# Optimization experiments

Hardware: AMD Instinct MI355X
Metric: run time of the kernel (lower is better)

Reference implementation:

```python
import jax, jax.numpy as jnp
import numpy as np

N_USERS = 200_000
N_ITEMS = 100_000
EMB = 64
N_EDGES = 5_000_000
N_LAYERS = 3


def setup_inputs() -> dict:
    key = jax.random.key(0)
    k1, k2, k3, k4, k5 = jax.random.split(key, 5)
    emb_user = jax.random.normal(k1, (N_USERS, EMB), dtype=jnp.float32) * 0.1
    emb_item = jax.random.normal(k2, (N_ITEMS, EMB), dtype=jnp.float32) * 0.1
    n_nodes = N_USERS + N_ITEMS
    edge_row = jax.random.randint(k3, (N_EDGES,), 0, n_nodes, dtype=jnp.int32)
    edge_col = jax.random.randint(k4, (N_EDGES,), 0, n_nodes, dtype=jnp.int32)
    # normalized adjacency values (positive, < 1), stand-in for D^-1/2 A D^-1/2
    edge_val = jax.random.uniform(k5, (N_EDGES,), dtype=jnp.float32)
    return {"emb_user": emb_user, "emb_item": emb_item,
            "edge_val": edge_val, "edge_row": edge_row, "edge_col": edge_col}


def reference(emb_user, emb_item, edge_val, edge_row, edge_col):
    n_users = emb_user.shape[0]
    n_nodes = n_users + emb_item.shape[0]
    # 0th-layer embedding matrix: cat(user, item)  [N, D]
    x = jnp.concatenate([emb_user, emb_item], axis=0)
    layers = [x]
    for _ in range(N_LAYERS):
        # SpMM: out[r] += val * x[c] for each edge (r, c)
        x = jax.ops.segment_sum(edge_val[:, None] * x[edge_col], edge_row,
                                num_segments=n_nodes)
        layers.append(x)
    # layer combination: mean over all layers
    agg = jnp.mean(jnp.stack(layers, axis=0), axis=0)
    return agg[:n_users], agg[n_users:]
```

## Files before the change

### kernel.cpp

```cpp
#include <hip/hip_runtime.h>

#define N_USERS 200000
#define N_ITEMS 100000
#define N_NODES 300000
#define EMB     64
#define N_EDGES 5000000

typedef float f32x4 __attribute__((ext_vector_type(4)));
typedef _Float16 f16;
typedef f16 f16x4 __attribute__((ext_vector_type(4)));

struct alignas(8) SRec { unsigned int rc; float val; };

#define BSHIFT 10
#define BROWS  (1 << BSHIFT)
#define NBUCK  ((N_NODES + BROWS - 1) >> BSHIFT)
#define CAP    20000
#define BIN_CHUNK 16384
#define BIN_THREADS 1024
#define COLMASK 0x7FFFFu
#define INIT_BLOCKS 512

__global__ __launch_bounds__(1024) void fused_init_bin_kernel(
    const float* __restrict__ user, const float* __restrict__ item,
    f16* __restrict__ x0,
    const int4* __restrict__ row4, const int4* __restrict__ col4,
    const float4* __restrict__ val4,
    int* __restrict__ bcursor, SRec* __restrict__ stage, int bin_blocks)
{
    int t = threadIdx.x;
    if ((int)blockIdx.x < bin_blocks) {
        __shared__ int hist[NBUCK];
        __shared__ int base_[NBUCK];
        const int Q = N_EDGES / 4;
        long q0 = (long)blockIdx.x * (BIN_CHUNK / 4);

        for (int k = t; k < NBUCK; k += BIN_THREADS) hist[k] = 0;
        __syncthreads();

        int4 ra[4];
        const bool full = (q0 + (BIN_CHUNK / 4) <= Q);
        if (full) {
            #pragma unroll
            for (int k = 0; k < 4; ++k)
                ra[k] = row4[q0 + k * BIN_THREADS + t];
            #pragma unroll
            for (int k = 0; k < 4; ++k) {
                atomicAdd(&hist[ra[k].x >> BSHIFT], 1);
                atomicAdd(&hist[ra[k].y >> BSHIFT], 1);
                atomicAdd(&hist[ra[k].z >> BSHIFT], 1);
                atomicAdd(&hist[ra[k].w >> BSHIFT], 1);
            }
        } else {
            #pragma unroll
            for (int k = 0; k < 4; ++k) {
                long q = q0 + k * BIN_THREADS + t;
                if (q < Q) {
                    ra[k] = row4[q];
                    atomicAdd(&hist[ra[k].x >> BSHIFT], 1);
                    atomicAdd(&hist[ra[k].y >> BSHIFT], 1);
                    atomicAdd(&hist[ra[k].z >> BSHIFT], 1);
                    atomicAdd(&hist[ra[k].w >> BSHIFT], 1);
                }
            }
        }
        __syncthreads();
        for (int k = t; k < NBUCK; k += BIN_THREADS) {
            int h = hist[k];
            base_[k] = h ? atomicAdd(&bcursor[k], h) : 0;
            hist[k] = 0;
        }
        __syncthreads();
        int4 c4[4]; float4 v4[4];
        if (full) {
            #pragma unroll
            for (int k = 0; k < 4; ++k) {
                c4[k] = col4[q0 + k * BIN_THREADS + t];
                v4[k] = val4[q0 + k * BIN_THREADS + t];
            }
        } else {
            #pragma unroll
            for (int k = 0; k < 4; ++k) {
                long q = q0 + k * BIN_THREADS + t;
                if (q < Q) { c4[k] = col4[q]; v4[k] = val4[q]; }
            }
        }
        #pragma unroll
        for (int k = 0; k < 4; ++k) {
            long q = q0 + k * BIN_THREADS + t;
            if (full || q < Q) {
                int   rr[4] = {ra[k].x, ra[k].y, ra[k].z, ra[k].w};
                int   cc[4] = {c4[k].x, c4[k].y, c4[k].z, c4[k].w};
                float vv[4] = {v4[k].x, v4[k].y, v4[k].z, v4[k].w};
                #pragma unroll
                for (int m = 0; m < 4; ++m) {
                    int b   = rr[m] >> BSHIFT;
                    int pos = base_[b] + atomicAdd(&hist[b], 1);
                    SRec s;
                    s.rc  = ((unsigned)(rr[m] & (BROWS - 1)) << 19)
                          | (unsigned)cc[m];
                    s.val = vv[m];
                    stage[(size_t)b * CAP + pos] = s;
                }
            }
        }
    } else {
        const int nu4 = N_USERS * EMB / 4;
        const int nt4 = N_NODES * EMB / 4;
        int i0 = ((int)blockIdx.x - bin_blocks) * BIN_THREADS + t;
        const int stride = INIT_BLOCKS * BIN_THREADS;
        for (int i = i0; i < nt4; i += stride) {
            float4 vv = (i < nu4) ? reinterpret_cast<const float4*>(user)[i]
                                  : reinterpret_cast<const float4*>(item)[i - nu4];
            f16x4 hx = {(f16)vv.x, (f16)vv.y, (f16)vv.z, (f16)vv.w};
            reinterpret_cast<f16x4*>(x0)[i] = hx;
        }
    }
}

__global__ __launch_bounds__(1024) void bucket_scan_scatter_kernel(
    const SRec* __restrict__ stage, const int* __restrict__ bsize,
    int* __restrict__ start, unsigned short* __restrict__ cnt16,
    int* __restrict__ pcol, f16* __restrict__ pval)
{
    __shared__ int cur[BROWS];
    __shared__ int sc[1024];
    __shared__ int lcol[CAP];
    __shared__ f16 lval[CAP];

    int b    = blockIdx.x;
    int t    = threadIdx.x;
    int row0 = b << BSHIFT;
    int rows = N_NODES - row0; if (rows > BROWS) rows = BROWS;

    const int  size = bsize[b];
    const int  base = b * CAP;
    const SRec* seg = stage + (size_t)b * CAP;

    cur[t] = 0;
    __syncthreads();

    for (int e = t; e < size; e += 1024)
        atomicAdd(&cur[seg[e].rc >> 19], 1);
    __syncthreads();

    int a = cur[t];
    sc[t] = a;
    __syncthreads();
    for (int ofs = 1; ofs < 1024; ofs <<= 1) {
        int v = (t >= ofs) ? sc[t - ofs] : 0;
        __syncthreads();
        sc[t] += v;
        __syncthreads();
    }
    int excl = sc[t] - a;
    cur[t] = excl;
    if (t < rows) {
        start[row0 + t] = base + excl;
        cnt16[row0 + t] = (unsigned short)a;
    }
    __syncthreads();

    for (int e = t; e < size; e += 1024) {
        SRec srec = seg[e];
        int idx = atomicAdd(&cur[srec.rc >> 19], 1);
        lcol[idx] = (int)(srec.rc & COLMASK);
        lval[idx] = (f16)srec.val;
    }
    __syncthreads();

    for (int i = t; i < size; i += 1024) pcol[base + i] = lcol[i];
    for (int i = t; i < size; i += 1024) pval[base + i] = lval[i];
}

__global__ __launch_bounds__(256, 4) void spmm_csr_kernel(
    const f16* __restrict__ x, const int* __restrict__ pcol,
    const f16* __restrict__ pval, const int* __restrict__ start,
    const unsigned short* __restrict__ cnt16,
    f16* __restrict__ y,
    const f16* __restrict__ xa, const f16* __restrict__ xb,
    float* __restrict__ out, int mode)
{
    int g = blockIdx.x * (256 / 16) + (threadIdx.x >> 4);
    if (g >= N_NODES) return;
    const int lane16 = threadIdx.x & 15;
    const int d      = lane16 * 4;
    const int gbase  = threadIdx.x & 48;

    int beg = start[g];
    int end = beg + cnt16[g];
    float4 acc = {0.f, 0.f, 0.f, 0.f};

    for (int jb = beg; jb < end; jb += 16) {
        int   mycol = 0; float myval = 0.f;
        if (jb + lane16 < end) {
            mycol = pcol[jb + lane16];
            myval = (float)pval[jb + lane16];
        }

        int   cols[16];
        float vals[16];
        #pragma unroll
        for (int k = 0; k < 16; ++k) {
            cols[k] = __shfl(mycol, gbase + k, 64);
            vals[k] = __shfl(myval, gbase + k, 64);
        }

        f16x4 xv[16];
        #pragma unroll
        for (int k = 0; k < 16; ++k) {
            xv[k] = *reinterpret_cast<const f16x4*>(
                x + (size_t)cols[k] * EMB + d);
        }

        #pragma unroll
        for (int k = 0; k < 16; ++k) {
            acc.x += vals[k] * (float)xv[k].x;
            acc.y += vals[k] * (float)xv[k].y;
            acc.z += vals[k] * (float)xv[k].z;
            acc.w += vals[k] * (float)xv[k].w;
        }
    }

    const size_t rofs = (size_t)g * EMB + d;
    if (mode == 0) {
        f16x4 hy = {(f16)acc.x, (f16)acc.y, (f16)acc.z, (f16)acc.w};
        *reinterpret_cast<f16x4*>(y + rofs) = hy;
    } else {
        f16x4 v0 = *reinterpret_cast<const f16x4*>(xa + rofs);
        f16x4 v1 = *reinterpret_cast<const f16x4*>(xb + rofs);
        f16x4 v2 = *reinterpret_cast<const f16x4*>(x  + rofs);
        f32x4 o;
        o.x = 0.25f * ((float)v0.x + (float)v1.x + (float)v2.x + acc.x);
        o.y = 0.25f * ((float)v0.y + (float)v1.y + (float)v2.y + acc.y);
        o.z = 0.25f * ((float)v0.z + (float)v1.z + (float)v2.z + acc.z);
        o.w = 0.25f * ((float)v0.w + (float)v1.w + (float)v2.w + acc.w);
        __builtin_nontemporal_store(o, reinterpret_cast<f32x4*>(out + rofs));
    }
}

__global__ __launch_bounds__(256) void init_kernel(
    const float* __restrict__ user, const float* __restrict__ item,
    float* __restrict__ x, float* __restrict__ out)
{
    const int nu4 = N_USERS * EMB / 4;
    const int nt4 = N_NODES * EMB / 4;
    int i = blockIdx.x * blockDim.x + threadIdx.x;
    if (i >= nt4) return;
    float4 v = (i < nu4) ? reinterpret_cast<const float4*>(user)[i]
                         : reinterpret_cast<const float4*>(item)[i - nu4];
    reinterpret_cast<float4*>(x)[i]   = v;
    reinterpret_cast<float4*>(out)[i] = v;
}

__global__ __launch_bounds__(256) void spmm_atomic_kernel(
    const float* __restrict__ x, const float* __restrict__ val,
    const int* __restrict__ row, const int* __restrict__ col,
    float* __restrict__ y)
{
    int t = blockIdx.x * blockDim.x + threadIdx.x;
    int e = t >> 4;
    if (e >= N_EDGES) return;
    int d = (t & 15) * 4;
    int   r = row[e];
    int   c = col[e];
    float v = val[e];
    float4 xv = *reinterpret_cast<const float4*>(x + c * EMB + d);
    float* yp = y + r * EMB + d;
    unsafeAtomicAdd(yp + 0, v * xv.x);
    unsafeAtomicAdd(yp + 1, v * xv.y);
    unsafeAtomicAdd(yp + 2, v * xv.z);
    unsafeAtomicAdd(yp + 3, v * xv.w);
}

__global__ __launch_bounds__(256) void addscale_kernel(
    const float* __restrict__ xl, float* __restrict__ out, float scale)
{
    const int nt4 = N_NODES * EMB / 4;
    int i = blockIdx.x * blockDim.x + threadIdx.x;
    if (i >= nt4) return;
    float4 a = reinterpret_cast<float4*>(out)[i];
    float4 b = reinterpret_cast<const float4*>(xl)[i];
    a.x = (a.x + b.x) * scale;
    a.y = (a.y + b.y) * scale;
    a.z = (a.z + b.z) * scale;
    a.w = (a.w + b.w) * scale;
    reinterpret_cast<float4*>(out)[i] = a;
}

extern "C" void kernel_launch(void* const* d_in, const int* in_sizes, int n_in,
                              void* d_out, int out_size, void* d_ws, size_t ws_size,
                              hipStream_t stream) {
    const float* emb_user = (const float*)d_in[0];
    const float* emb_item = (const float*)d_in[1];
    const float* edge_val = (const float*)d_in[2];
    const int*   edge_row = (const int*)d_in[3];
    const int*   edge_col = (const int*)d_in[4];
    float* out = (float*)d_out;

    const size_t node_elems = (size_t)N_NODES * EMB;
    char* ws = (char*)d_ws;

    const size_t off_bufA    = 0;
    const size_t off_bufB    = off_bufA + node_elems * sizeof(float);
    const size_t off_pcol    = off_bufB + node_elems * sizeof(float);
    const size_t off_pval    = off_pcol + (size_t)NBUCK * CAP * sizeof(int);
    const size_t off_start   = off_pval + (size_t)NBUCK * CAP * sizeof(f16);
    const size_t off_cnt16   = off_start + (N_NODES + 4) * sizeof(int);
    const size_t off_bcursor = off_cnt16 + (N_NODES + 4) * sizeof(unsigned short);
    const size_t needed      = off_bcursor + (NBUCK + 4) * sizeof(int);

    const int nt4       = N_NODES * EMB / 4;
    const int el_blocks = (nt4 + 255) / 256;
    const int e_blocks  = (N_EDGES + 255) / 256;

    static_assert((size_t)NBUCK * CAP * sizeof(SRec) <= (size_t)N_NODES * EMB * sizeof(float),
                  "stage must fit in bufB region");

    if (ws_size >= needed) {
        f16*  x0buf   = (f16*) (ws + off_bufA);
        f16*  x2buf   = (f16*) (ws + off_bufA) + node_elems;
        f16*  x1buf   = (f16*) (ws + off_bufB);
        int*  pcol    = (int*) (ws + off_pcol);
        f16*  pval    = (f16*) (ws + off_pval);
        int*  start   = (int*) (ws + off_start);
        unsigned short* cnt16 = (unsigned short*)(ws + off_cnt16);
        int*  bcursor = (int*) (ws + off_bcursor);
        SRec* stage   = (SRec*)(ws + off_bufB);

        hipMemsetAsync(bcursor, 0, (NBUCK + 4) * sizeof(int), stream);

        const int bin_blocks = (N_EDGES + BIN_CHUNK - 1) / BIN_CHUNK;
        fused_init_bin_kernel<<<bin_blocks + INIT_BLOCKS, BIN_THREADS, 0, stream>>>(
            emb_user, emb_item, x0buf,
            (const int4*)edge_row, (const int4*)edge_col, (const float4*)edge_val,
            bcursor, stage, bin_blocks);

        bucket_scan_scatter_kernel<<<NBUCK, 1024, 0, stream>>>(
            stage, bcursor, start, cnt16, pcol, pval);

        const int row_blocks = (N_NODES + 15) / 16;
        spmm_csr_kernel<<<row_blocks, 256, 0, stream>>>(
            x0buf, pcol, pval, start, cnt16, x1buf, nullptr, nullptr, nullptr, 0);
        spmm_csr_kernel<<<row_blocks, 256, 0, stream>>>(
            x1buf, pcol, pval, start, cnt16, x2buf, nullptr, nullptr, nullptr, 0);
        spmm_csr_kernel<<<row_blocks, 256, 0, stream>>>(
            x2buf, pcol, pval, start, cnt16, nullptr, x0buf, x1buf, out, 1);
    } else {
        float* fbufA = (float*)(ws + off_bufA);
        float* fbufB = (float*)(ws + off_bufB);
        init_kernel<<<el_blocks, 256, 0, stream>>>(emb_user, emb_item, fbufA, out);
        const int ew_blocks = (N_EDGES * 16 + 255) / 256;
        float* cur = fbufA;
        float* nxt = fbufB;
        for (int layer = 0; layer < 3; ++layer) {
            hipMemsetAsync(nxt, 0, node_elems * sizeof(float), stream);
            spmm_atomic_kernel<<<ew_blocks, 256, 0, stream>>>(
                cur, edge_val, edge_row, edge_col, nxt);
            addscale_kernel<<<el_blocks, 256, 0, stream>>>(
                nxt, out, (layer == 2) ? 0.25f : 1.0f);
            float* tmp = cur; cur = nxt; nxt = tmp;
        }
    }
}
```

Baseline: 549.6 us.

## Stage binned edges in shared memory for coalesced bucket writes

Measured after the change: 530.9 us. 3.4% less time.

```diff
diff --git a/kernel.cpp b/kernel.cpp
--- a/kernel.cpp
+++ b/kernel.cpp
@@ -30,10 +30,16 @@
 {
     int t = threadIdx.x;
     if ((int)blockIdx.x < bin_blocks) {
-        __shared__ int hist[NBUCK];
-        __shared__ int base_[NBUCK];
+        __shared__ int  hist[NBUCK];
+        __shared__ int  lstart[NBUCK + 1];
+        __shared__ int  gbase[NBUCK];
+        __shared__ int  sc[512];
+        __shared__ SRec sbuf[BIN_CHUNK];
+
         const int Q = N_EDGES / 4;
         long q0 = (long)blockIdx.x * (BIN_CHUNK / 4);
+        int  csize = N_EDGES - (int)(q0 * 4);
+        if (csize > BIN_CHUNK) csize = BIN_CHUNK;
 
         for (int k = t; k < NBUCK; k += BIN_THREADS) hist[k] = 0;
         __syncthreads();
@@ -65,12 +71,26 @@
             }
         }
         __syncthreads();
-        for (int k = t; k < NBUCK; k += BIN_THREADS) {
-            int h = hist[k];
-            base_[k] = h ? atomicAdd(&bcursor[k], h) : 0;
-            hist[k] = 0;
-        }
-        __syncthreads();
+
+        int v = (t < NBUCK) ? hist[t] : 0;
+        if (t < 512) sc[t] = v;
+        __syncthreads();
+        for (int ofs = 1; ofs < 512; ofs <<= 1) {
+            int u = 0;
+            if (t < 512 && t >= ofs) u = sc[t - ofs];
+            __syncthreads();
+            if (t < 512) sc[t] += u;
+            __syncthreads();
+        }
+        if (t < NBUCK) lstart[t] = sc[t] - v;
+        if (t == NBUCK - 1) lstart[NBUCK] = sc[t];
+        __syncthreads();
+        if (t < NBUCK) {
+            gbase[t] = v ? atomicAdd(&bcursor[t], v) : 0;
+            hist[t]  = lstart[t];
+        }
+        __syncthreads();
+
         int4 c4[4]; float4 v4[4];
         if (full) {
             #pragma unroll
@@ -95,14 +115,24 @@
                 #pragma unroll
                 for (int m = 0; m < 4; ++m) {
                     int b   = rr[m] >> BSHIFT;
-                    int pos = base_[b] + atomicAdd(&hist[b], 1);
+                    int idx = atomicAdd(&hist[b], 1);
                     SRec s;
                     s.rc  = ((unsigned)(rr[m] & (BROWS - 1)) << 19)
                           | (unsigned)cc[m];
                     s.val = vv[m];
-                    stage[(size_t)b * CAP + pos] = s;
+                    sbuf[idx] = s;
                 }
             }
+        }
+        __syncthreads();
+
+        for (int i = t; i < csize; i += BIN_THREADS) {
+            int lo = 0, hi = NBUCK - 1;
+            while (lo < hi) {
+                int mid = (lo + hi + 1) >> 1;
+                if (lstart[mid] <= i) lo = mid; else hi = mid - 1;
+            }
+            stage[(size_t)lo * CAP + gbase[lo] + (i - lstart[lo])] = sbuf[i];
         }
     } else {
         const int nu4 = N_USERS * EMB / 4;
```

## Locally sort edges in shared memory before coalesced bucket staging writes

Applied to the files above, without the earlier changes.

Measured after the change: 524.9 us. -4.5%, faster.

```diff
diff --git a/kernel.cpp b/kernel.cpp
--- a/kernel.cpp
+++ b/kernel.cpp
@@ -10,142 +10,152 @@
 typedef _Float16 f16;
 typedef f16 f16x4 __attribute__((ext_vector_type(4)));
 
-struct alignas(8) SRec { unsigned int rc; float val; };
-
-#define BSHIFT 10
-#define BROWS  (1 << BSHIFT)
-#define NBUCK  ((N_NODES + BROWS - 1) >> BSHIFT)
-#define CAP    20000
-#define BIN_CHUNK 16384
-#define BIN_THREADS 1024
+#define NBUCK  256
+#define BROWS  1172
+#define CAP    20800
 #define COLMASK 0x7FFFFu
-#define INIT_BLOCKS 512
+
+#define BIN_CHUNK 19532
+#define BIN_Q     (BIN_CHUNK / 4)
 
 __global__ __launch_bounds__(1024) void fused_init_bin_kernel(
     const float* __restrict__ user, const float* __restrict__ item,
     f16* __restrict__ x0,
     const int4* __restrict__ row4, const int4* __restrict__ col4,
     const float4* __restrict__ val4,
-    int* __restrict__ bcursor, SRec* __restrict__ stage, int bin_blocks)
-{
-    int t = threadIdx.x;
-    if ((int)blockIdx.x < bin_blocks) {
-        __shared__ int hist[NBUCK];
-        __shared__ int base_[NBUCK];
-        const int Q = N_EDGES / 4;
-        long q0 = (long)blockIdx.x * (BIN_CHUNK / 4);
-
-        for (int k = t; k < NBUCK; k += BIN_THREADS) hist[k] = 0;
+    int* __restrict__ bcursor,
+    unsigned int* __restrict__ stage_rc, f16* __restrict__ stage_val)
+{
+    __shared__ unsigned int lrc[BIN_CHUNK];
+    __shared__ f16          lv[BIN_CHUNK];
+    __shared__ int hist[NBUCK];
+    __shared__ int lstart[NBUCK + 1];
+    __shared__ int gbase[NBUCK];
+    __shared__ int sc[NBUCK];
+
+    const int t = threadIdx.x;
+    const int b = blockIdx.x;
+    const int Q    = N_EDGES / 4;
+    const int q0   = b * BIN_Q;
+    int qend = q0 + BIN_Q; if (qend > Q) qend = Q;
+    const int csize = (qend - q0) * 4;
+
+    for (int k = t; k < NBUCK; k += 1024) hist[k] = 0;
+    __syncthreads();
+
+    int4 ra[5]; bool ok[5];
+    #pragma unroll
+    for (int k = 0; k < 5; ++k) {
+        int q = q0 + k * 1024 + t;
+        ok[k] = (q < qend);
+        if (ok[k]) ra[k] = row4[q];
+    }
+    #pragma unroll
+    for (int k = 0; k < 5; ++k) {
+        if (ok[k]) {
+            atomicAdd(&hist[ra[k].x / BROWS], 1);
+            atomicAdd(&hist[ra[k].y / BROWS], 1);
+            atomicAdd(&hist[ra[k].z / BROWS], 1);
+            atomicAdd(&hist[ra[k].w / BROWS], 1);
+        }
+    }
+    __syncthreads();
+
+    if (t < NBUCK) sc[t] = hist[t];
+    __syncthreads();
+    for (int ofs = 1; ofs < NBUCK; ofs <<= 1) {
+        int u = 0;
+        if (t < NBUCK && t >= ofs) u = sc[t - ofs];
         __syncthreads();
-
-        int4 ra[4];
-        const bool full = (q0 + (BIN_CHUNK / 4) <= Q);
-        if (full) {
+        if (t < NBUCK) sc[t] += u;
+        __syncthreads();
+    }
+    if (t < NBUCK) {
+        int v  = hist[t];
+        int ex = sc[t] - v;
+        lstart[t] = ex;
+        gbase[t]  = v ? atomicAdd(&bcursor[t], v) : 0;
+        hist[t]   = ex;
+    }
+    if (t == 0) lstart[NBUCK] = csize;
+    __syncthreads();
+
+    int4 c4[5]; float4 v4[5];
+    #pragma unroll
+    for (int k = 0; k < 5; ++k) {
+        int q = q0 + k * 1024 + t;
+        if (ok[k]) { c4[k] = col4[q]; v4[k] = val4[q]; }
+    }
+    #pragma unroll
+    for (int k = 0; k < 5; ++k) {
+        if (ok[k]) {
+            int   rr[4] = {ra[k].x, ra[k].y, ra[k].z, ra[k].w};
+            int   cc[4] = {c4[k].x, c4[k].y, c4[k].z, c4[k].w};
+            float vv[4] = {v4[k].x, v4[k].y, v4[k].z, v4[k].w};
             #pragma unroll
-            for (int k = 0; k < 4; ++k)
-                ra[k] = row4[q0 + k * BIN_THREADS + t];
-            #pragma unroll
-            for (int k = 0; k < 4; ++k) {
-                atomicAdd(&hist[ra[k].x >> BSHIFT], 1);
-                atomicAdd(&hist[ra[k].y >> BSHIFT], 1);
-                atomicAdd(&hist[ra[k].z >> BSHIFT], 1);
-                atomicAdd(&hist[ra[k].w >> BSHIFT], 1);
+            for (int m = 0; m < 4; ++m) {
+                int bb    = rr[m] / BROWS;
+                int local = rr[m] - bb * BROWS;
+                int idx   = atomicAdd(&hist[bb], 1);
+                lrc[idx]  = ((unsigned)local << 19) | (unsigned)cc[m];
+                lv[idx]   = (f16)vv[m];
             }
-        } else {
-            #pragma unroll
-            for (int k = 0; k < 4; ++k) {
-                long q = q0 + k * BIN_THREADS + t;
-                if (q < Q) {
-                    ra[k] = row4[q];
-                    atomicAdd(&hist[ra[k].x >> BSHIFT], 1);
-                    atomicAdd(&hist[ra[k].y >> BSHIFT], 1);
-                    atomicAdd(&hist[ra[k].z >> BSHIFT], 1);
-                    atomicAdd(&hist[ra[k].w >> BSHIFT], 1);
-                }
-            }
-        }
-        __syncthreads();
-        for (int k = t; k < NBUCK; k += BIN_THREADS) {
-            int h = hist[k];
-            base_[k] = h ? atomicAdd(&bcursor[k], h) : 0;
-            hist[k] = 0;
-        }
-        __syncthreads();
-        int4 c4[4]; float4 v4[4];
-        if (full) {
-            #pragma unroll
-            for (int k = 0; k < 4; ++k) {
-                c4[k] = col4[q0 + k * BIN_THREADS + t];
-                v4[k] = val4[q0 + k * BIN_THREADS + t];
-            }
-        } else {
-            #pragma unroll
-            for (int k = 0; k < 4; ++k) {
-                long q = q0 + k * BIN_THREADS + t;
-                if (q < Q) { c4[k] = col4[q]; v4[k] = val4[q]; }
-            }
-        }
-        #pragma unroll
-        for (int k = 0; k < 4; ++k) {
-            long q = q0 + k * BIN_THREADS + t;
-            if (full || q < Q) {
-                int   rr[4] = {ra[k].x, ra[k].y, ra[k].z, ra[k].w};
-                int   cc[4] = {c4[k].x, c4[k].y, c4[k].z, c4[k].w};
-                float vv[4] = {v4[k].x, v4[k].y, v4[k].z, v4[k].w};
-                #pragma unroll
-                for (int m = 0; m < 4; ++m) {
-                    int b   = rr[m] >> BSHIFT;
-                    int pos = base_[b] + atomicAdd(&hist[b], 1);
-                    SRec s;
-                    s.rc  = ((unsigned)(rr[m] & (BROWS - 1)) << 19)
-                          | (unsigned)cc[m];
-                    s.val = vv[m];
-                    stage[(size_t)b * CAP + pos] = s;
-                }
-            }
-        }
-    } else {
-        const int nu4 = N_USERS * EMB / 4;
-        const int nt4 = N_NODES * EMB / 4;
-        int i0 = ((int)blockIdx.x - bin_blocks) * BIN_THREADS + t;
-        const int stride = INIT_BLOCKS * BIN_THREADS;
-        for (int i = i0; i < nt4; i += stride) {
-            float4 vv = (i < nu4) ? reinterpret_cast<const float4*>(user)[i]
-                                  : reinterpret_cast<const float4*>(item)[i - nu4];
-            f16x4 hx = {(f16)vv.x, (f16)vv.y, (f16)vv.z, (f16)vv.w};
-            reinterpret_cast<f16x4*>(x0)[i] = hx;
-        }
+        }
+    }
+    __syncthreads();
+
+    for (int i = t; i < csize; i += 1024) {
+        int lo = 0, hi = NBUCK - 1;
+        while (lo < hi) {
+            int mid = (lo + hi + 1) >> 1;
+            if (lstart[mid] <= i) lo = mid; else hi = mid - 1;
+        }
+        size_t gp = (size_t)lo * CAP + gbase[lo] + (i - lstart[lo]);
+        stage_rc[gp]  = lrc[i];
+        stage_val[gp] = lv[i];
+    }
+
+    const int nu4 = N_USERS * EMB / 4;
+    const int nt4 = N_NODES * EMB / 4;
+    for (int i = b * 1024 + t; i < nt4; i += NBUCK * 1024) {
+        float4 vv = (i < nu4) ? reinterpret_cast<const float4*>(user)[i]
+                              : reinterpret_cast<const float4*>(item)[i - nu4];
+        f16x4 hx = {(f16)vv.x, (f16)vv.y, (f16)vv.z, (f16)vv.w};
+        reinterpret_cast<f16x4*>(x0)[i] = hx;
     }
 }
 
 __global__ __launch_bounds__(1024) void bucket_scan_scatter_kernel(
-    const SRec* __restrict__ stage, const int* __restrict__ bsize,
+    const unsigned int* __restrict__ stage_rc, const f16* __restrict__ stage_val,
+    const int* __restrict__ bsize,
     int* __restrict__ start, unsigned short* __restrict__ cnt16,
     int* __restrict__ pcol, f16* __restrict__ pval)
 {
-    __shared__ int cur[BROWS];
+    __shared__ int cur[BROWS + 2];
     __shared__ int sc[1024];
     __shared__ int lcol[CAP];
     __shared__ f16 lval[CAP];
 
     int b    = blockIdx.x;
     int t    = threadIdx.x;
-    int row0 = b << BSHIFT;
+    int row0 = b * BROWS;
     int rows = N_NODES - row0; if (rows > BROWS) rows = BROWS;
 
-    const int  size = bsize[b];
-    const int  base = b * CAP;
-    const SRec* seg = stage + (size_t)b * CAP;
-
-    cur[t] = 0;
+    const int size = bsize[b];
+    const int base = b * CAP;
+    const unsigned int* seg_rc = stage_rc  + (size_t)b * CAP;
+    const f16*          seg_v  = stage_val + (size_t)b * CAP;
+
+    for (int i = t; i < BROWS; i += 1024) cur[i] = 0;
     __syncthreads();
 
     for (int e = t; e < size; e += 1024)
-        atomicAdd(&cur[seg[e].rc >> 19], 1);
-    __syncthreads();
-
-    int a = cur[t];
-    sc[t] = a;
+        atomicAdd(&cur[seg_rc[e] >> 19], 1);
+    __syncthreads();
+
+    int a0 = 0, a1 = 0, s01 = 0;
+    if (t < 586) { a0 = cur[2 * t]; a1 = cur[2 * t + 1]; s01 = a0 + a1; }
+    sc[t] = s01;
     __syncthreads();
     for (int ofs = 1; ofs < 1024; ofs <<= 1) {
         int v = (t >= ofs) ? sc[t - ofs] : 0;
@@ -153,19 +163,21 @@
         sc[t] += v;
         __syncthreads();
     }
-    int excl = sc[t] - a;
-    cur[t] = excl;
-    if (t < rows) {
-        start[row0 + t] = base + excl;
-        cnt16[row0 + t] = (unsigned short)a;
+    if (t < 586) {
+        int ex = sc[t] - s01;
+        cur[2 * t]     = ex;
+        cur[2 * t + 1] = ex + a0;
+        int r0 = 2 * t, r1 = 2 * t + 1;
+        if (r0 < rows) { start[row0 + r0] = base + ex;      cnt16[row0 + r0] = (unsigned short)a0; }
+        if (r1 < rows) { start[row0 + r1] = base + ex + a0; cnt16[row0 + r1] = (unsigned short)a1; }
     }
     __syncthreads();
 
     for (int e = t; e < size; e += 1024) {
-        SRec srec = seg[e];
-        int idx = atomicAdd(&cur[srec.rc >> 19], 1);
-        lcol[idx] = (int)(srec.rc & COLMASK);
-        lval[idx] = (f16)srec.val;
+        unsigned int rc = seg_rc[e];
+        int idx = atomicAdd(&cur[rc >> 19], 1);
+        lcol[idx] = (int)(rc & COLMASK);
+        lval[idx] = seg_v[e];
     }
     __syncthreads();
 
@@ -299,45 +311,46 @@
     float* out = (float*)d_out;
 
     const size_t node_elems = (size_t)N_NODES * EMB;
+    const size_t SEG        = (size_t)NBUCK * CAP;
     char* ws = (char*)d_ws;
 
     const size_t off_bufA    = 0;
     const size_t off_bufB    = off_bufA + node_elems * sizeof(float);
     const size_t off_pcol    = off_bufB + node_elems * sizeof(float);
-    const size_t off_pval    = off_pcol + (size_t)NBUCK * CAP * sizeof(int);
-    const size_t off_start   = off_pval + (size_t)NBUCK * CAP * sizeof(f16);
+    const size_t off_pval    = off_pcol + SEG * sizeof(int);
+    const size_t off_start   = off_pval + SEG * sizeof(f16);
     const size_t off_cnt16   = off_start + (N_NODES + 4) * sizeof(int);
     const size_t off_bcursor = off_cnt16 + (N_NODES + 4) * sizeof(unsigned short);
     const size_t needed      = off_bcursor + (NBUCK + 4) * sizeof(int);
 
     const int nt4       = N_NODES * EMB / 4;
     const int el_blocks = (nt4 + 255) / 256;
-    const int e_blocks  = (N_EDGES + 255) / 256;
-
-    static_assert((size_t)NBUCK * CAP * sizeof(SRec) <= (size_t)N_NODES * EMB * sizeof(float),
+
+    static_assert(SEG * 6 <= (size_t)N_NODES * EMB * sizeof(float),
                   "stage must fit in bufB region");
+    static_assert((size_t)NBUCK * BROWS >= N_NODES, "buckets must cover rows");
 
     if (ws_size >= needed) {
         f16*  x0buf   = (f16*) (ws + off_bufA);
         f16*  x2buf   = (f16*) (ws + off_bufA) + node_elems;
         f16*  x1buf   = (f16*) (ws + off_bufB);
+        unsigned int* stage_rc  = (unsigned int*)(ws + off_bufB);
+        f16*          stage_val = (f16*)(ws + off_bufB + SEG * sizeof(int));
         int*  pcol    = (int*) (ws + off_pcol);
         f16*  pval    = (f16*) (ws + off_pval);
         int*  start   = (int*) (ws + off_start);
         unsigned short* cnt16 = (unsigned short*)(ws + off_cnt16);
         int*  bcursor = (int*) (ws + off_bcursor);
-        SRec* stage   = (SRec*)(ws + off_bufB);
 
         hipMemsetAsync(bcursor, 0, (NBUCK + 4) * sizeof(int), stream);
 
-        const int bin_blocks = (N_EDGES + BIN_CHUNK - 1) / BIN_CHUNK;
-        fused_init_bin_kernel<<<bin_blocks + INIT_BLOCKS, BIN_THREADS, 0, stream>>>(
+        fused_init_bin_kernel<<<NBUCK, 1024, 0, stream>>>(
             emb_user, emb_item, x0buf,
             (const int4*)edge_row, (const int4*)edge_col, (const float4*)edge_val,
-            bcursor, stage, bin_blocks);
+            bcursor, stage_rc, stage_val);
 
         bucket_scan_scatter_kernel<<<NBUCK, 1024, 0, stream>>>(
-            stage, bcursor, start, cnt16, pcol, pval);
+            stage_rc, stage_val, bcursor, start, cnt16, pcol, pval);
 
         const int row_blocks = (N_NODES + 15) / 16;
         spmm_csr_kernel<<<row_blocks, 256, 0, stream>>>(
```
